# Kernel tuning notes

Hardware: AMD Instinct MI355X
Metric: run time of the kernel (lower is better)

## Reference

```python
import jax, jax.numpy as jnp
import numpy as np


def conv3x3(x, w):
    # x: [B,C,H,W], w: [O,I,3,3], stride 1, pad 1, no bias
    return jax.lax.conv_general_dilated(
        x, w, window_strides=(1, 1), padding=[(1, 1), (1, 1)],
        dimension_numbers=("NCHW", "OIHW", "NCHW"))


def deform_conv2d(x, offset, w):
    """torchvision-style DeformConv2d: k=3, stride=1, pad=1, dilation=1,
    1 offset group, no bias. x:[B,C,H,W], offset:[B,18,H,W] (dy,dx pairs
    per kernel tap, k = kh*3+kw), w:[O,C,3,3]. Zero padding outside."""
    B, C, H, W = x.shape
    K = 9
    dy = offset[:, 0::2]  # [B,9,H,W]
    dx = offset[:, 1::2]
    kh = (jnp.arange(K) // 3 - 1).astype(x.dtype)[None, :, None, None]
    kw = (jnp.arange(K) % 3 - 1).astype(x.dtype)[None, :, None, None]
    hh = jnp.arange(H, dtype=x.dtype)[None, None, :, None]
    ww = jnp.arange(W, dtype=x.dtype)[None, None, None, :]
    py = hh + kh + dy  # sampling y coord, [B,9,H,W]
    px = ww + kw + dx
    y0 = jnp.floor(py)
    x0 = jnp.floor(px)
    wy = py - y0
    wx = px - x0
    x_hwc = jnp.transpose(x, (0, 2, 3, 1))  # [B,H,W,C]
    b_idx = jnp.arange(B)[:, None, None, None]

    def gather(yi, xi):
        valid = (yi >= 0) & (yi <= H - 1) & (xi >= 0) & (xi <= W - 1)
        yc = jnp.clip(yi, 0, H - 1).astype(jnp.int32)
        xc = jnp.clip(xi, 0, W - 1).astype(jnp.int32)
        v = x_hwc[b_idx, yc, xc]  # [B,9,H,W,C]
        return v * valid[..., None].astype(x.dtype)

    v00 = gather(y0, x0)
    v01 = gather(y0, x0 + 1)
    v10 = gather(y0 + 1, x0)
    v11 = gather(y0 + 1, x0 + 1)
    wy = wy[..., None]
    wx = wx[..., None]
    sampled = (v00 * (1 - wy) * (1 - wx) + v01 * (1 - wy) * wx
               + v10 * wy * (1 - wx) + v11 * wy * wx)  # [B,9,H,W,C]
    wk = w.reshape(w.shape[0], w.shape[1], K)  # [O,C,9]
    return jnp.einsum("bkhwc,ock->bohw", sampled, wk)


def setup_inputs() -> dict:
    key = jax.random.key(0)
    ks = jax.random.split(key, 6)
    B, C, H, W = 2, 128, 128, 128
    s = 0.05  # small init so learned offsets stay in a realistic range
    return {
        "input_features": jax.random.normal(ks[0], (B, C, H, W), jnp.float32),
        "reference_features": jax.random.normal(ks[1], (B, C, H, W), jnp.float32),
        "w_est1": jax.random.normal(ks[2], (C, 2 * C, 3, 3), jnp.float32) * s,
        "w_est2": jax.random.normal(ks[3], (C, C, 3, 3), jnp.float32) * s,
        "w_off": jax.random.normal(ks[4], (18, C, 3, 3), jnp.float32) * s,
        "w_def": jax.random.normal(ks[5], (C, C, 3, 3), jnp.float32) * s,
    }


def reference(input_features, reference_features, w_est1, w_est2, w_off, w_def):
    # concat input+reference features along channel dim
    feat = jnp.concatenate([input_features, reference_features], axis=1)  # [B,2C,H,W]
    # dynamic offset estimator: 2-layer 3x3 conv stack 2C->C->C with ReLU
    est = jax.nn.relu(conv3x3(feat, w_est1))
    est = jax.nn.relu(conv3x3(est, w_est2))
    # offset head: C -> 2*9 offsets per pixel
    offset = conv3x3(est, w_off)  # [B,18,H,W]
    # deformable conv over the reference features
    return deform_conv2d(reference_features, offset, w_def)
```

## Files before the change

kernel.cpp:

```cpp
#include <hip/hip_runtime.h>

typedef _Float16 f16;
typedef __attribute__((ext_vector_type(8))) _Float16 f16x8;
typedef __attribute__((ext_vector_type(4))) float f32x4;


__device__ __forceinline__ void g2l16(const void* g, void* l) {
  __builtin_amdgcn_global_load_lds((const __attribute__((address_space(1))) void*)g,
                                   (__attribute__((address_space(3))) void*)l, 16, 0, 0);
}

__device__ __forceinline__ void pack_conv(const float* __restrict__ src, f16* __restrict__ dst,
                                          long idx, int C) {
  int ci3 = idx & 7;
  int g = (idx >> 3) & 3;
  long t = idx >> 5;
  int o = (int)(t & 63); t >>= 6;
  int kx = (int)(t % 3); t /= 3;
  int nb = (int)(t & 1); t >>= 1;
  int nkc = C >> 5;
  int cc = (int)(t % nkc);
  int ky = (int)(t / nkc);
  int og = nb * 64 + o;
  int c = (cc << 5) + ((g ^ ((o >> 1) & 3)) << 3) + ci3;
  dst[idx] = (f16)src[(((size_t)og * C + c) * 3 + ky) * 3 + kx];
}

__device__ __forceinline__ void halo_zero(f16* __restrict__ buf, long e) {
  int c = (int)(e & 127);
  long t = e >> 7;
  int b = (int)(t / 516);
  int p = (int)(t % 516);
  int y, x;
  if (p < 130)      { y = 0;   x = p; }
  else if (p < 260) { y = 129; x = p - 130; }
  else if (p < 388) { x = 0;   y = p - 259; }
  else              { x = 129; y = p - 387; }
  buf[((size_t)(b * 130 + y) * 130 + x) * 128 + c] = (f16)0.f;
}

__global__ __launch_bounds__(256) void init_k(const float* __restrict__ x, const float* __restrict__ ref,
                                              const float* __restrict__ w1, const float* __restrict__ w2,
                                              const float* __restrict__ woff, const float* __restrict__ wdef,
                                              f16* __restrict__ W1p, f16* __restrict__ W2p,
                                              f16* __restrict__ Woffp, f16* __restrict__ Wdefp,
                                              f16* __restrict__ xP, f16* __restrict__ refP,
                                              f16* __restrict__ est1, f16* __restrict__ est2) {
  __shared__ __align__(16) f16 T[64][40];
  int tid = threadIdx.x;
  if (blockIdx.x < 4096) {
    int bi = blockIdx.x;
    int row = bi & 255, wseg = (bi >> 8) & 1, chunk = bi >> 9;
    int b = row >> 7, h = row & 127;
    int w0 = wseg * 64;
    const float* src = (chunk < 4) ? x : ref;
    f16* dstp = (chunk < 4) ? xP : refP;
    int c0 = (chunk & 3) * 32;
#pragma unroll
    for (int i = 0; i < 2; ++i) {
      int idx = tid + i * 256;
      int c = idx >> 4, g = idx & 15;
      const float4 v = *(const float4*)(src + (((size_t)(b * 128 + c0 + c)) * 128 + h) * 128 + w0 + g * 4);
      T[g * 4 + 0][c] = (f16)v.x;
      T[g * 4 + 1][c] = (f16)v.y;
      T[g * 4 + 2][c] = (f16)v.z;
      T[g * 4 + 3][c] = (f16)v.w;
    }
    __syncthreads();
    int w = tid >> 2, g = tid & 3;
    f16x8 o = *(const f16x8*)&T[w][g * 8];
    *(f16x8*)(dstp + ((size_t)(b * 130 + h + 1) * 130 + w0 + w + 1) * 128 + c0 + g * 8) = o;
    return;
  }
  long idx = (long)(blockIdx.x - 4096) * 256 + tid;
  if (idx < 294912) { pack_conv(w1, W1p, idx, 256); return; }
  idx -= 294912;
  if (idx < 147456) { pack_conv(w2, W2p, idx, 128); return; }
  idx -= 147456;
  if (idx < 36864) {
    int ci3 = (int)(idx & 7);
    int g = (int)((idx >> 3) & 3);
    int o = (int)((idx >> 5) & 31);
    int t2 = (int)(idx >> 10);
    int kx = t2 % 3; t2 /= 3;
    int cc = t2 & 3, ky = t2 >> 2;
    int c = (cc << 5) + ((g ^ ((o >> 1) & 3)) << 3) + ci3;
    Woffp[idx] = (o < 18) ? (f16)woff[(((size_t)o * 128 + c) * 3 + ky) * 3 + kx] : (f16)0.f;
    return;
  }
  idx -= 36864;
  if (idx < 147456) {
    int j = (int)(idx & 7);
    int ln = (int)((idx >> 3) & 63);
    int ofr = (int)((idx >> 9) & 7);
    int cc = (int)((idx >> 12) & 3);
    int t = (int)(idx >> 14);
    int o = ofr * 16 + (ln & 15);
    int c = cc * 32 + (ln >> 4) * 8 + j;
    Wdefp[idx] = (f16)wdef[(((size_t)o * 128 + c) * 3 + t / 3) * 3 + t % 3];
    return;
  }
  idx -= 147456;
  if (idx < 132096) { halo_zero(xP, idx); return; }
  idx -= 132096;
  if (idx < 132096) { halo_zero(refP, idx); return; }
  idx -= 132096;
  if (idx < 132096) { halo_zero(est1, idx); return; }
  idx -= 132096;
  if (idx < 132096) halo_zero(est2, idx);
}

template <int NKC>
__global__ __launch_bounds__(256, 3) void conv_k(const f16* __restrict__ src0,
                                                 const f16* __restrict__ src1,
                                                 const f16* __restrict__ Wp,
                                                 f16* __restrict__ dst) {
  constexpr int S = 3 * NKC;
  const int row = blockIdx.x, nb = blockIdx.y;
  const int b = row >> 7, h = row & 127;
  __shared__ __align__(16) f16 As[2][130][32];
  __shared__ __align__(16) f16 Bs[2][3][64][32];
  const int tid = threadIdx.x;
  const int lane = tid & 63, wave = tid >> 6;
  const int l16 = lane & 15, quad = lane >> 4;
  const int wmB = wave * 32;
  f32x4 acc[2][4] = {};

  auto stage = [&](int s, int buf) {
    int ky = s / NKC, cc = s % NKC;
    const f16* sp = (NKC == 8 && cc >= 4) ? src1 : src0;
    int c0 = (NKC == 8 ? (cc & 3) : cc) * 32;
    const f16* abase = sp + ((size_t)(b * 130 + h + ky) * 130) * 128 + c0;
#pragma unroll
    for (int rr = 0; rr < 2; ++rr) {
      int ch = rr * 256 + tid;
      int xx = ch >> 2, g = ch & 3;
      g2l16(abase + (size_t)xx * 128 + ((g ^ ((xx >> 1) & 3)) << 3),
            (char*)&As[buf][0][0] + ch * 16);
    }
    if (tid < 8) {
      int ch = 512 + tid;
      int xx = ch >> 2, g = ch & 3;
      g2l16(abase + (size_t)xx * 128 + ((g ^ ((xx >> 1) & 3)) << 3),
            (char*)&As[buf][0][0] + ch * 16);
    }
    const f16* bbase = Wp + (size_t)((ky * NKC + cc) * 2 + nb) * (3 * 64 * 32);
#pragma unroll
    for (int rr = 0; rr < 3; ++rr) {
      int ch = rr * 256 + tid;
      g2l16(bbase + (size_t)ch * 8, (char*)&Bs[buf][0][0][0] + ch * 16);
    }
  };

  stage(0, 0);
  __syncthreads();
  for (int s = 0; s < S; ++s) {
    if (s + 1 < S) stage(s + 1, (s + 1) & 1);
    const int buf = s & 1;
#pragma unroll
    for (int kx = 0; kx < 3; ++kx) {
      f16x8 bf[4];
#pragma unroll
      for (int j = 0; j < 4; ++j) {
        int o = j * 16 + l16;
        bf[j] = *(const f16x8*)&Bs[buf][kx][o][(quad ^ ((o >> 1) & 3)) << 3];
      }
#pragma unroll
      for (int i = 0; i < 2; ++i) {
        int xx = wmB + i * 16 + l16 + kx;
        f16x8 a = *(const f16x8*)&As[buf][xx][(quad ^ ((xx >> 1) & 3)) << 3];
#pragma unroll
        for (int j = 0; j < 4; ++j)
          acc[i][j] = __builtin_amdgcn_mfma_f32_16x16x32_f16(a, bf[j], acc[i][j], 0, 0, 0);
      }
    }
    __syncthreads();
  }
#pragma unroll
  for (int i = 0; i < 2; ++i)
#pragma unroll
    for (int j = 0; j < 4; ++j) {
      int o = nb * 64 + j * 16 + l16;
#pragma unroll
      for (int rr = 0; rr < 4; ++rr) {
        int m = wmB + i * 16 + quad * 4 + rr;
        float v = fmaxf(acc[i][j][rr], 0.f);
        dst[((size_t)(b * 130 + h + 1) * 130 + m + 1) * 128 + o] = (f16)v;
      }
    }
}

__global__ __launch_bounds__(256, 3) void conv_off_k(const f16* __restrict__ src,
                                                     const f16* __restrict__ Wp,
                                                     float* __restrict__ dst) {
  const int row = blockIdx.x;
  const int b = row >> 7, h = row & 127;
  __shared__ __align__(16) f16 As[2][130][32];
  __shared__ __align__(16) f16 Bs[2][3][32][32];
  const int tid = threadIdx.x;
  const int lane = tid & 63, wave = tid >> 6;
  const int l16 = lane & 15, quad = lane >> 4;
  const int wmB = wave * 32;
  f32x4 acc[2][2] = {};

  auto stage = [&](int s, int buf) {
    int ky = s >> 2, cc = s & 3;
    const f16* abase = src + ((size_t)(b * 130 + h + ky) * 130) * 128 + cc * 32;
#pragma unroll
    for (int rr = 0; rr < 2; ++rr) {
      int ch = rr * 256 + tid;
      int xx = ch >> 2, g = ch & 3;
      g2l16(abase + (size_t)xx * 128 + ((g ^ ((xx >> 1) & 3)) << 3),
            (char*)&As[buf][0][0] + ch * 16);
    }
    if (tid < 8) {
      int ch = 512 + tid;
      int xx = ch >> 2, g = ch & 3;
      g2l16(abase + (size_t)xx * 128 + ((g ^ ((xx >> 1) & 3)) << 3),
            (char*)&As[buf][0][0] + ch * 16);
    }
    const f16* bbase = Wp + (size_t)(ky * 4 + cc) * (3 * 32 * 32);
    {
      g2l16(bbase + (size_t)tid * 8, (char*)&Bs[buf][0][0][0] + tid * 16);
      if (tid < 128) {
        int ch = 256 + tid;
        g2l16(bbase + (size_t)ch * 8, (char*)&Bs[buf][0][0][0] + ch * 16);
      }
    }
  };

  stage(0, 0);
  __syncthreads();
  for (int s = 0; s < 12; ++s) {
    if (s + 1 < 12) stage(s + 1, (s + 1) & 1);
    const int buf = s & 1;
#pragma unroll
    for (int kx = 0; kx < 3; ++kx) {
      f16x8 bf[2];
#pragma unroll
      for (int j = 0; j < 2; ++j) {
        int o = j * 16 + l16;
        bf[j] = *(const f16x8*)&Bs[buf][kx][o][(quad ^ ((o >> 1) & 3)) << 3];
      }
#pragma unroll
      for (int i = 0; i < 2; ++i) {
        int xx = wmB + i * 16 + l16 + kx;
        f16x8 a = *(const f16x8*)&As[buf][xx][(quad ^ ((xx >> 1) & 3)) << 3];
#pragma unroll
        for (int j = 0; j < 2; ++j)
          acc[i][j] = __builtin_amdgcn_mfma_f32_16x16x32_f16(a, bf[j], acc[i][j], 0, 0, 0);
      }
    }
    __syncthreads();
  }
#pragma unroll
  for (int i = 0; i < 2; ++i)
#pragma unroll
    for (int j = 0; j < 2; ++j)
#pragma unroll
      for (int rr = 0; rr < 4; ++rr) {
        int m = wmB + i * 16 + quad * 4 + rr;
        int o = j * 16 + l16;
        dst[((size_t)row * 128 + m) * 32 + o] = acc[i][j][rr];
      }
}

__global__ __launch_bounds__(256, 3) void deform_k(const f16* __restrict__ refP,
                                                   const float* __restrict__ offb,
                                                   const f16* __restrict__ Wdefp,
                                                   float* __restrict__ out) {
  const int row = blockIdx.x, tile = blockIdx.y;
  const int b = row >> 7, h = row & 127;
  __shared__ __align__(16) f16 Ss[2][64][128];
  __shared__ int4 meta[9][64];
  const int tid = threadIdx.x;
  const int lane = tid & 63, wave = tid >> 6;
  const int l16 = lane & 15, quad = lane >> 4;

  for (int e = tid; e < 576; e += 256) {
    int t = e >> 6, p = e & 63;
    int wg = tile * 64 + p;
    const float2 d = *(const float2*)(offb + ((size_t)row * 128 + wg) * 32 + 2 * t);
    float py = (float)(h + t / 3 - 1) + d.x;
    float px = (float)(wg + t % 3 - 1) + d.y;
    float fy = floorf(py), fx = floorf(px);
    meta[t][p] = make_int4((int)fy, (int)fx, __float_as_int(py - fy), __float_as_int(px - fx));
  }

  auto sample = [&](int t, int buf) {
    const int p = tid >> 2, cg = tid & 3;
    int4 mt = meta[t][p];
    int yp = mt.x + 1, xp = mt.y + 1;
    float wy = __int_as_float(mt.z), wx = __int_as_float(mt.w);
    bool y0v = (unsigned)yp < 130u, y1v = (unsigned)(yp + 1) < 130u;
    bool x0v = (unsigned)xp < 130u, x1v = (unsigned)(xp + 1) < 130u;
    int cy0 = y0v ? yp : 0, cy1 = y1v ? yp + 1 : 0;
    int cx0 = x0v ? xp : 0, cx1 = x1v ? xp + 1 : 0;
    float u0 = (1.f - wy) * (y0v ? 1.f : 0.f), u1 = wy * (y1v ? 1.f : 0.f);
    float s0 = (1.f - wx) * (x0v ? 1.f : 0.f), s1 = wx * (x1v ? 1.f : 0.f);
    f16 h00 = (f16)(u0 * s0), h01 = (f16)(u0 * s1);
    f16 h10 = (f16)(u1 * s0), h11 = (f16)(u1 * s1);
    const size_t bb = (size_t)b * 130;
    const f16* p00 = refP + ((bb + cy0) * 130 + cx0) * 128 + cg * 32;
    const f16* p01 = refP + ((bb + cy0) * 130 + cx1) * 128 + cg * 32;
    const f16* p10 = refP + ((bb + cy1) * 130 + cx0) * 128 + cg * 32;
    const f16* p11 = refP + ((bb + cy1) * 130 + cx1) * 128 + cg * 32;
    f16x8 v00[4], v01[4], v10[4], v11[4];
#pragma unroll
    for (int q = 0; q < 4; ++q) {
      v00[q] = *(const f16x8*)(p00 + q * 8);
      v01[q] = *(const f16x8*)(p01 + q * 8);
      v10[q] = *(const f16x8*)(p10 + q * 8);
      v11[q] = *(const f16x8*)(p11 + q * 8);
    }
#pragma unroll
    for (int q = 0; q < 4; ++q) {
      f16x8 rb = v00[q] * h00 + v01[q] * h01 + v10[q] * h10 + v11[q] * h11;
      int c = cg * 4 + q;
      *(f16x8*)&Ss[buf][p][(c ^ (p & 7)) << 3] = rb;
    }
  };

  f32x4 acc[2][4] = {};
  __syncthreads();
  sample(0, 0);
  __syncthreads();
  for (int t = 0; t < 9; ++t) {
    f16x8 af[4][2];
#pragma unroll
    for (int cc = 0; cc < 4; ++cc)
#pragma unroll
      for (int i = 0; i < 2; ++i)
        af[cc][i] = *(const f16x8*)(Wdefp +
            ((((size_t)t * 4 + cc) * 8 + wave * 2 + i) * 64 + lane) * 8);
    if (t < 8) sample(t + 1, (t + 1) & 1);
    const int buf = t & 1;
#pragma unroll
    for (int cc = 0; cc < 4; ++cc) {
      f16x8 bf[4];
#pragma unroll
      for (int j = 0; j < 4; ++j) {
        int p = j * 16 + l16;
        bf[j] = *(const f16x8*)&Ss[buf][p][((cc * 4 + quad) ^ (p & 7)) << 3];
      }
#pragma unroll
      for (int i = 0; i < 2; ++i)
#pragma unroll
        for (int j = 0; j < 4; ++j)
          acc[i][j] = __builtin_amdgcn_mfma_f32_16x16x32_f16(af[cc][i], bf[j], acc[i][j], 0, 0, 0);
    }
    __syncthreads();
  }
#pragma unroll
  for (int i = 0; i < 2; ++i)
#pragma unroll
    for (int rr = 0; rr < 4; ++rr) {
      int o = wave * 32 + i * 16 + quad * 4 + rr;
#pragma unroll
      for (int j = 0; j < 4; ++j) {
        int wg = tile * 64 + j * 16 + l16;
        out[((size_t)(b * 128 + o) * 128 + h) * 128 + wg] = acc[i][j][rr];
      }
    }
}

extern "C" void kernel_launch(void* const* d_in, const int* in_sizes, int n_in,
                              void* d_out, int out_size, void* d_ws, size_t ws_size,
                              hipStream_t stream) {
  const float* x = (const float*)d_in[0];
  const float* ref = (const float*)d_in[1];
  const float* w1 = (const float*)d_in[2];
  const float* w2 = (const float*)d_in[3];
  const float* woff = (const float*)d_in[4];
  const float* wdef = (const float*)d_in[5];
  float* out = (float*)d_out;
  char* ws = (char*)d_ws;
  f16* xP = (f16*)(ws + 0);
  f16* refP = (f16*)(ws + 8652800);
  f16* est1 = (f16*)(ws + 17305600);
  f16* est2 = (f16*)(ws + 25958400);
  float* offb = (float*)(ws + 34611200);
  f16* W1p = (f16*)(ws + 38805504);
  f16* W2p = (f16*)(ws + 39395328);
  f16* Woffp = (f16*)(ws + 39690240);
  f16* Wdefp = (f16*)(ws + 39763968);

  init_k<<<dim3(8608), 256, 0, stream>>>(x, ref, w1, w2, woff, wdef,
                                         W1p, W2p, Woffp, Wdefp, xP, refP, est1, est2);
  conv_k<8><<<dim3(256, 2), 256, 0, stream>>>(xP, refP, W1p, est1);
  conv_k<4><<<dim3(256, 2), 256, 0, stream>>>(est1, est1, W2p, est2);
  conv_off_k<<<dim3(256), 256, 0, stream>>>(est2, Woffp, offb);
  deform_k<<<dim3(256, 2), 256, 0, stream>>>(refP, offb, Wdefp, out);
}
```

Baseline: 180.7 us.

## Compute all 128 output channels per block in conv kernels with 2x2 wave tiling

The two estimator conv kernels now compute the full 128 output channels for one image row per block, instead of splitting the channels across two blocks. The four waves are arranged as a 2x2 grid of 64x64 tiles, and the weight packing layout is changed to match. This avoids loading the same input row into LDS twice and raises the MFMA-to-LDS-read ratio. In exchange the grid drops from 512 to 256 blocks, which is about one block per CU and may leave parallelism thin. Per-block LDS and register use also grow, and launch bounds drop to 1 block per CU.

```diff
diff --git a/kernel.cpp b/kernel.cpp
--- a/kernel.cpp
+++ b/kernel.cpp
@@ -15,15 +15,13 @@
   int ci3 = idx & 7;
   int g = (idx >> 3) & 3;
   long t = idx >> 5;
-  int o = (int)(t & 63); t >>= 6;
+  int o = (int)(t & 127); t >>= 7;
   int kx = (int)(t % 3); t /= 3;
-  int nb = (int)(t & 1); t >>= 1;
   int nkc = C >> 5;
   int cc = (int)(t % nkc);
   int ky = (int)(t / nkc);
-  int og = nb * 64 + o;
   int c = (cc << 5) + ((g ^ ((o >> 1) & 3)) << 3) + ci3;
-  dst[idx] = (f16)src[(((size_t)og * C + c) * 3 + ky) * 3 + kx];
+  dst[idx] = (f16)src[(((size_t)o * C + c) * 3 + ky) * 3 + kx];
 }
 
 __device__ __forceinline__ void halo_zero(f16* __restrict__ buf, long e) {
@@ -111,20 +109,21 @@
 }
 
 template <int NKC>
-__global__ __launch_bounds__(256, 3) void conv_k(const f16* __restrict__ src0,
+__global__ __launch_bounds__(256, 1) void conv_k(const f16* __restrict__ src0,
                                                  const f16* __restrict__ src1,
                                                  const f16* __restrict__ Wp,
                                                  f16* __restrict__ dst) {
   constexpr int S = 3 * NKC;
-  const int row = blockIdx.x, nb = blockIdx.y;
+  const int row = blockIdx.x;
   const int b = row >> 7, h = row & 127;
   __shared__ __align__(16) f16 As[2][130][32];
-  __shared__ __align__(16) f16 Bs[2][3][64][32];
+  __shared__ __align__(16) f16 Bs[2][3][128][32];
   const int tid = threadIdx.x;
   const int lane = tid & 63, wave = tid >> 6;
   const int l16 = lane & 15, quad = lane >> 4;
-  const int wmB = wave * 32;
-  f32x4 acc[2][4] = {};
+  const int wm = (wave & 1) * 64;
+  const int wn = (wave >> 1) * 64;
+  f32x4 acc[4][4] = {};
 
   auto stage = [&](int s, int buf) {
     int ky = s / NKC, cc = s % NKC;
@@ -144,9 +143,9 @@
       g2l16(abase + (size_t)xx * 128 + ((g ^ ((xx >> 1) & 3)) << 3),
             (char*)&As[buf][0][0] + ch * 16);
     }
-    const f16* bbase = Wp + (size_t)((ky * NKC + cc) * 2 + nb) * (3 * 64 * 32);
-#pragma unroll
-    for (int rr = 0; rr < 3; ++rr) {
+    const f16* bbase = Wp + (size_t)(ky * NKC + cc) * (3 * 128 * 32);
+#pragma unroll
+    for (int rr = 0; rr < 6; ++rr) {
       int ch = rr * 256 + tid;
       g2l16(bbase + (size_t)ch * 8, (char*)&Bs[buf][0][0][0] + ch * 16);
     }
@@ -159,31 +158,33 @@
     const int buf = s & 1;
 #pragma unroll
     for (int kx = 0; kx < 3; ++kx) {
-      f16x8 bf[4];
+      f16x8 bf[4], af[4];
 #pragma unroll
       for (int j = 0; j < 4; ++j) {
-        int o = j * 16 + l16;
+        int o = wn + j * 16 + l16;
         bf[j] = *(const f16x8*)&Bs[buf][kx][o][(quad ^ ((o >> 1) & 3)) << 3];
       }
 #pragma unroll
-      for (int i = 0; i < 2; ++i) {
-        int xx = wmB + i * 16 + l16 + kx;
-        f16x8 a = *(const f16x8*)&As[buf][xx][(quad ^ ((xx >> 1) & 3)) << 3];
+      for (int i = 0; i < 4; ++i) {
+        int xx = wm + i * 16 + l16 + kx;
+        af[i] = *(const f16x8*)&As[buf][xx][(quad ^ ((xx >> 1) & 3)) << 3];
+      }
+#pragma unroll
+      for (int i = 0; i < 4; ++i)
 #pragma unroll
         for (int j = 0; j < 4; ++j)
-          acc[i][j] = __builtin_amdgcn_mfma_f32_16x16x32_f16(a, bf[j], acc[i][j], 0, 0, 0);
-      }
+          acc[i][j] = __builtin_amdgcn_mfma_f32_16x16x32_f16(af[i], bf[j], acc[i][j], 0, 0, 0);
     }
     __syncthreads();
   }
 #pragma unroll
-  for (int i = 0; i < 2; ++i)
+  for (int i = 0; i < 4; ++i)
 #pragma unroll
     for (int j = 0; j < 4; ++j) {
-      int o = nb * 64 + j * 16 + l16;
+      int o = wn + j * 16 + l16;
 #pragma unroll
       for (int rr = 0; rr < 4; ++rr) {
-        int m = wmB + i * 16 + quad * 4 + rr;
+        int m = wm + i * 16 + quad * 4 + rr;
         float v = fmaxf(acc[i][j][rr], 0.f);
         dst[((size_t)(b * 130 + h + 1) * 130 + m + 1) * 128 + o] = (f16)v;
       }
@@ -387,8 +388,8 @@
 
   init_k<<<dim3(8608), 256, 0, stream>>>(x, ref, w1, w2, woff, wdef,
                                          W1p, W2p, Woffp, Wdefp, xP, refP, est1, est2);
-  conv_k<8><<<dim3(256, 2), 256, 0, stream>>>(xP, refP, W1p, est1);
-  conv_k<4><<<dim3(256, 2), 256, 0, stream>>>(est1, est1, W2p, est2);
+  conv_k<8><<<dim3(256), 256, 0, stream>>>(xP, refP, W1p, est1);
+  conv_k<4><<<dim3(256), 256, 0, stream>>>(est1, est1, W2p, est2);
   conv_off_k<<<dim3(256), 256, 0, stream>>>(est2, Woffp, offb);
   deform_k<<<dim3(256, 2), 256, 0, stream>>>(refP, offb, Wdefp, out);
 }
```

After: 189.7 us. 1.05x slower.
